# Optimization experiments

Measured on AMD Instinct MI355X. Metric: run time of the kernel, lower is better.

The kernel has to match this reference:

```python
import jax, jax.numpy as jnp
import numpy as np


def _gather_nbrs(feats, idx):
    # feats: [C, N], idx: [N, k] -> [C, N, k]
    return feats[:, idx]


def pointconv_dw(xyz, feats, idx, w_pos, b_pos, w_out, b_out):
    """Depthwise point conv: per-channel weights from relative neighbor coords.
    xyz: [B,3,N], feats: [B,C,N], idx: [B,N,k] -> [B,C_out,N]
    """
    nbr_xyz = jax.vmap(_gather_nbrs)(xyz, idx)            # [B,3,N,k]
    rel = nbr_xyz - xyz[:, :, :, None]                    # relative positions
    w = jnp.einsum('cd,bdnk->bcnk', w_pos, rel) + b_pos[None, :, None, None]
    g = jax.vmap(_gather_nbrs)(feats, idx)                # [B,C,N,k]
    agg = jnp.sum(w * g, axis=-1)                         # [B,C,N] depthwise reduce over k
    return jnp.einsum('oc,bcn->bon', w_out, agg) + b_out[None, :, None]


def setup_inputs() -> dict:
    key = jax.random.key(0)
    ks = jax.random.split(key, 16)
    B, N, K = 2, 65536, 4
    IN, HID = 64, 64
    C = HID + IN
    s = 0.02
    inp = {
        'xyz': jax.random.normal(ks[0], (B, 3, N), jnp.float32),
        'h': jax.random.normal(ks[1], (B, HID, N), jnp.float32),
        'x': jax.random.normal(ks[2], (B, IN, N), jnp.float32),
        'knn_indices': jax.random.randint(ks[3], (B, N, K), 0, N, jnp.int32),
    }
    names = ['z', 'r', 'q']
    for i, nm in enumerate(names):
        inp[f'w{nm}_pos'] = s * jax.random.normal(ks[4 + 4 * i], (C, 3), jnp.float32)
        inp[f'b{nm}_pos'] = jnp.zeros((C,), jnp.float32)
        inp[f'w{nm}_out'] = s * jax.random.normal(ks[5 + 4 * i], (HID, C), jnp.float32)
        inp[f'b{nm}_out'] = jnp.zeros((HID,), jnp.float32)
    return inp


def reference(xyz, h, x, knn_indices,
              wz_pos, bz_pos, wz_out, bz_out,
              wr_pos, br_pos, wr_out, br_out,
              wq_pos, bq_pos, wq_out, bq_out):
    hx = jnp.concatenate([h, x], axis=1)                  # [B, HID+IN, N]
    z = jax.nn.sigmoid(pointconv_dw(xyz, hx, knn_indices, wz_pos, bz_pos, wz_out, bz_out))
    r = jax.nn.sigmoid(pointconv_dw(xyz, hx, knn_indices, wr_pos, br_pos, wr_out, br_out))
    rhx = jnp.concatenate([r * h, x], axis=1)
    q = jnp.tanh(pointconv_dw(xyz, rhx, knn_indices, wq_pos, bq_pos, wq_out, bq_out))
    return (1.0 - z) * h + z * q
```

## Files before the change

### kernel.cpp

```cpp
#include <hip/hip_runtime.h>

#define NPTS 65536
#define BATCH 2
#define CCH 128
#define HIDC 64
#define LDA 136
#define ZLD 72

typedef unsigned short u16;
typedef __bf16 bf16_t;
typedef bf16_t bf16x8 __attribute__((ext_vector_type(8)));
typedef float f32x4 __attribute__((ext_vector_type(4)));

__device__ __forceinline__ u16 f2bf(float f){
  union { float f; unsigned u; } v; v.f = f;
  unsigned r = v.u + 0x7FFFu + ((v.u >> 16) & 1u);
  return (u16)(r >> 16);
}
__device__ __forceinline__ float bf2f(u16 u){
  union { unsigned u; float f; } v; v.u = ((unsigned)u) << 16; return v.f;
}
__device__ __forceinline__ float sigmoidf_(float v){ return 1.f/(1.f+__expf(-v)); }
__device__ __forceinline__ float tanhf_(float v){
  v = fminf(10.f, fmaxf(-10.f, v));
  float e = __expf(2.f*v);
  return (e-1.f)/(e+1.f);
}

__global__ __launch_bounds__(256) void kprep(const float* __restrict__ wz,
    const float* __restrict__ wr, const float* __restrict__ wq, u16* __restrict__ o){
  int i = blockIdx.x*256 + threadIdx.x;
  const float* s = (i < 8192) ? wz : ((i < 16384) ? wr : wq);
  o[i] = f2bf(s[i & 8191]);
}

__global__ __launch_bounds__(256) void k_pack(const float* __restrict__ h,
    const float* __restrict__ x, u16* __restrict__ hxT, u16* __restrict__ rhxT){
  int pn = blockIdx.x*256 + threadIdx.x;
  int b = pn >> 16;
  size_t fb = (size_t)b*HIDC*NPTS + (pn & 65535);
  size_t ob = (size_t)pn * CCH;
  u16 tmp[8];
  for (int c8 = 0; c8 < 8; ++c8){
    #pragma unroll
    for (int i = 0; i < 8; ++i) tmp[i] = f2bf(h[fb + (size_t)(c8*8+i)*NPTS]);
    uint4 v; __builtin_memcpy(&v, tmp, 16);
    *(uint4*)(hxT + ob + c8*8) = v;
  }
  for (int c8 = 0; c8 < 8; ++c8){
    #pragma unroll
    for (int i = 0; i < 8; ++i) tmp[i] = f2bf(x[fb + (size_t)(c8*8+i)*NPTS]);
    uint4 v; __builtin_memcpy(&v, tmp, 16);
    *(uint4*)(hxT + ob + 64 + c8*8) = v;
    *(uint4*)(rhxT + ob + 64 + c8*8) = v;
  }
}

__global__ __launch_bounds__(256) void k_zr(
    const float* __restrict__ xyz, const float* __restrict__ h,
    const int* __restrict__ knn,
    const float* __restrict__ wz_pos, const float* __restrict__ bz_pos,
    const float* __restrict__ bz_out,
    const float* __restrict__ wr_pos, const float* __restrict__ br_pos,
    const float* __restrict__ br_out,
    const u16* __restrict__ wzb, const u16* __restrict__ wrb,
    const u16* __restrict__ hxT, u16* __restrict__ rhxT, u16* __restrict__ z_ws)
{
  __shared__ __align__(16) u16 aggzT[64*LDA];
  __shared__ __align__(16) u16 aggrT[64*LDA];
  __shared__ __align__(16) u16 zst[64*ZLD];
  __shared__ float4 relk[256];
  __shared__ int jlds[256];
  __shared__ float4 wpz[128];
  __shared__ float4 wpr[128];

  int tid = threadIdx.x; int lane = tid & 63; int wv = tid >> 6;
  int bid = blockIdx.x; int b = bid >> 10; int n0 = (bid & 1023) << 6;
  size_t bN = (size_t)b * NPTS;

  {
    int p = tid >> 2, k = tid & 3;
    int j = knn[((bN + n0 + p) << 2) + k];
    jlds[tid] = j;
    const float* xb = xyz + (size_t)b*3*NPTS;
    float cx = xb[n0+p], cy = xb[NPTS + n0+p], cz = xb[2*NPTS + n0+p];
    relk[tid] = make_float4(xb[j]-cx, xb[NPTS+j]-cy, xb[2*NPTS+j]-cz, 0.f);
  }
  if (tid < 128){
    wpz[tid] = make_float4(wz_pos[tid*3], wz_pos[tid*3+1], wz_pos[tid*3+2], bz_pos[tid]);
  } else {
    int c = tid - 128;
    wpr[c] = make_float4(wr_pos[c*3], wr_pos[c*3+1], wr_pos[c*3+2], br_pos[c]);
  }
  __syncthreads();

  const u16* hxTb = hxT + (bN << 7);
  for (int i = 0; i < 32; ++i){
    int t = (i << 2) | wv;
    int p = t >> 1; int c = ((t & 1) << 6) | lane;
    float4 wz4 = wpz[c], wr4 = wpr[c];
    float az = 0.f, ar = 0.f;
    #pragma unroll
    for (int k = 0; k < 4; ++k){
      int j = jlds[(p << 2) | k];
      float g = bf2f(hxTb[((size_t)j << 7) | c]);
      float4 r = relk[(p << 2) | k];
      az += (wz4.w + wz4.x*r.x + wz4.y*r.y + wz4.z*r.z) * g;
      ar += (wr4.w + wr4.x*r.x + wr4.y*r.y + wr4.z*r.z) * g;
    }
    aggzT[p*LDA + c] = f2bf(az);
    aggrT[p*LDA + c] = f2bf(ar);
  }
  __syncthreads();

  int l15 = lane & 15, quad = lane >> 4;
  bf16x8 Az[4], Ar[4];
  #pragma unroll
  for (int s = 0; s < 4; ++s){
    Az[s] = *(const bf16x8*)(wzb + ((wv*16 + l15)*128 + s*32 + quad*8));
    Ar[s] = *(const bf16x8*)(wrb + ((wv*16 + l15)*128 + s*32 + quad*8));
  }
  f32x4 zero4 = {0.f,0.f,0.f,0.f};
  f32x4 accz[4], accr[4];
  #pragma unroll
  for (int nt = 0; nt < 4; ++nt){ accz[nt] = zero4; accr[nt] = zero4; }
  #pragma unroll
  for (int nt = 0; nt < 4; ++nt){
    #pragma unroll
    for (int s = 0; s < 4; ++s){
      bf16x8 bz = *(const bf16x8*)(aggzT + ((nt*16 + l15)*LDA + s*32 + quad*8));
      accz[nt] = __builtin_amdgcn_mfma_f32_16x16x32_bf16(Az[s], bz, accz[nt], 0, 0, 0);
    }
    #pragma unroll
    for (int s = 0; s < 4; ++s){
      bf16x8 br = *(const bf16x8*)(aggrT + ((nt*16 + l15)*LDA + s*32 + quad*8));
      accr[nt] = __builtin_amdgcn_mfma_f32_16x16x32_bf16(Ar[s], br, accr[nt], 0, 0, 0);
    }
  }
  __syncthreads();

  #pragma unroll
  for (int nt = 0; nt < 4; ++nt){
    #pragma unroll
    for (int reg = 0; reg < 4; ++reg){
      int o = (wv << 4) | (quad << 2) | reg;
      int p = (nt << 4) | l15;
      float zf = sigmoidf_(accz[nt][reg] + bz_out[o]);
      float rf = sigmoidf_(accr[nt][reg] + br_out[o]);
      float hv = h[(size_t)(b*HIDC + o)*NPTS + n0 + p];
      zst[o*ZLD + p] = f2bf(zf);
      aggzT[p*LDA + o] = f2bf(rf * hv);
    }
  }
  __syncthreads();

  for (int t = tid; t < 512; t += 256){
    int p = t >> 3, ch = (t & 7) << 3;
    uint4 v = *(const uint4*)(aggzT + p*LDA + ch);
    *(uint4*)(rhxT + ((bN + n0 + p) << 7) + ch) = v;
  }
  for (int t = tid; t < 512; t += 256){
    int o = t >> 3, ch = (t & 7) << 3;
    uint4 v = *(const uint4*)(zst + o*ZLD + ch);
    *(uint4*)(z_ws + (size_t)(b*HIDC + o)*NPTS + n0 + ch) = v;
  }
}

__global__ __launch_bounds__(256) void k_q(
    const float* __restrict__ xyz, const float* __restrict__ h,
    const int* __restrict__ knn,
    const float* __restrict__ wq_pos, const float* __restrict__ bq_pos,
    const float* __restrict__ bq_out,
    const u16* __restrict__ wqb, const u16* __restrict__ rhxT,
    const u16* __restrict__ z_ws, float* __restrict__ out)
{
  __shared__ __align__(16) u16 aggT[64*LDA];
  __shared__ float4 relk[256];
  __shared__ int jlds[256];
  __shared__ float4 wpq[128];

  int tid = threadIdx.x; int lane = tid & 63; int wv = tid >> 6;
  int bid = blockIdx.x; int b = bid >> 10; int n0 = (bid & 1023) << 6;
  size_t bN = (size_t)b * NPTS;

  {
    int p = tid >> 2, k = tid & 3;
    int j = knn[((bN + n0 + p) << 2) + k];
    jlds[tid] = j;
    const float* xb = xyz + (size_t)b*3*NPTS;
    float cx = xb[n0+p], cy = xb[NPTS + n0+p], cz = xb[2*NPTS + n0+p];
    relk[tid] = make_float4(xb[j]-cx, xb[NPTS+j]-cy, xb[2*NPTS+j]-cz, 0.f);
  }
  if (tid < 128){
    wpq[tid] = make_float4(wq_pos[tid*3], wq_pos[tid*3+1], wq_pos[tid*3+2], bq_pos[tid]);
  }
  __syncthreads();

  const u16* rhxTb = rhxT + (bN << 7);
  for (int i = 0; i < 32; ++i){
    int t = (i << 2) | wv;
    int p = t >> 1; int c = ((t & 1) << 6) | lane;
    float4 wq4 = wpq[c];
    float aq = 0.f;
    #pragma unroll
    for (int k = 0; k < 4; ++k){
      int j = jlds[(p << 2) | k];
      float g = bf2f(rhxTb[((size_t)j << 7) | c]);
      float4 r = relk[(p << 2) | k];
      aq += (wq4.w + wq4.x*r.x + wq4.y*r.y + wq4.z*r.z) * g;
    }
    aggT[p*LDA + c] = f2bf(aq);
  }
  __syncthreads();

  int l15 = lane & 15, quad = lane >> 4;
  bf16x8 Aq[4];
  #pragma unroll
  for (int s = 0; s < 4; ++s)
    Aq[s] = *(const bf16x8*)(wqb + ((wv*16 + l15)*128 + s*32 + quad*8));
  f32x4 zero4 = {0.f,0.f,0.f,0.f};
  f32x4 acc[4];
  #pragma unroll
  for (int nt = 0; nt < 4; ++nt) acc[nt] = zero4;
  #pragma unroll
  for (int nt = 0; nt < 4; ++nt){
    #pragma unroll
    for (int s = 0; s < 4; ++s){
      bf16x8 bq = *(const bf16x8*)(aggT + ((nt*16 + l15)*LDA + s*32 + quad*8));
      acc[nt] = __builtin_amdgcn_mfma_f32_16x16x32_bf16(Aq[s], bq, acc[nt], 0, 0, 0);
    }
  }

  #pragma unroll
  for (int nt = 0; nt < 4; ++nt){
    #pragma unroll
    for (int reg = 0; reg < 4; ++reg){
      int o = (wv << 4) | (quad << 2) | reg;
      int p = (nt << 4) | l15;
      size_t idx = (size_t)(b*HIDC + o)*NPTS + n0 + p;
      float qf = tanhf_(acc[nt][reg] + bq_out[o]);
      float zf = bf2f(z_ws[idx]);
      float hv = h[idx];
      out[idx] = (1.f - zf)*hv + zf*qf;
    }
  }
}

extern "C" void kernel_launch(void* const* d_in, const int* in_sizes, int n_in,
                              void* d_out, int out_size, void* d_ws, size_t ws_size,
                              hipStream_t stream){
  const float* xyz    = (const float*)d_in[0];
  const float* h      = (const float*)d_in[1];
  const float* x      = (const float*)d_in[2];
  const int*   knn    = (const int*)d_in[3];
  const float* wz_pos = (const float*)d_in[4];
  const float* bz_pos = (const float*)d_in[5];
  const float* wz_out = (const float*)d_in[6];
  const float* bz_out = (const float*)d_in[7];
  const float* wr_pos = (const float*)d_in[8];
  const float* br_pos = (const float*)d_in[9];
  const float* wr_out = (const float*)d_in[10];
  const float* br_out = (const float*)d_in[11];
  const float* wq_pos = (const float*)d_in[12];
  const float* bq_pos = (const float*)d_in[13];
  const float* wq_out = (const float*)d_in[14];
  const float* bq_out = (const float*)d_in[15];
  float* out = (float*)d_out;

  u16* ws   = (u16*)d_ws;
  u16* hxT  = ws;
  u16* rhxT = hxT + (size_t)BATCH*NPTS*CCH;
  u16* z_ws = rhxT + (size_t)BATCH*NPTS*CCH;
  u16* wbf  = z_ws + (size_t)BATCH*HIDC*NPTS;

  kprep<<<96, 256, 0, stream>>>(wz_out, wr_out, wq_out, wbf);
  k_pack<<<512, 256, 0, stream>>>(h, x, hxT, rhxT);
  k_zr<<<2048, 256, 0, stream>>>(xyz, h, knn, wz_pos, bz_pos, bz_out,
      wr_pos, br_pos, br_out, wbf, wbf + 8192, hxT, rhxT, z_ws);
  k_q<<<2048, 256, 0, stream>>>(xyz, h, knn, wq_pos, bq_pos, bq_out,
      wbf + 16384, rhxT, z_ws, out);
}
```

Baseline: 269.1 us.

## Fold position weights into output GEMM and vectorize neighbor gathers

Rewrites the depthwise position-weighted aggregation algebraically. Each point now keeps four moments per channel (sum of g, and x/y/z-weighted sums of g), giving a K=512 extended B matrix. The position coefficients are folded into the output weights in a prep kernel, so the per-channel weight computation becomes part of the MFMA GEMM. Gathers are vectorized as 16-byte loads per neighbor, the pack kernel transposes through LDS with coalesced float4 reads, and tiles shrink to 32 points per block with 4-block occupancy hints. The cost is four times more MFMA K-work and an extra bf16 rounding on the moments.

```diff
diff --git a/kernel.cpp b/kernel.cpp
--- a/kernel.cpp
+++ b/kernel.cpp
@@ -4,10 +4,12 @@
 #define BATCH 2
 #define CCH 128
 #define HIDC 64
-#define LDA 136
-#define ZLD 72
+#define PPB 32
+#define LDB 520
+#define PLD 136
 
 typedef unsigned short u16;
+typedef unsigned int u32;
 typedef __bf16 bf16_t;
 typedef bf16_t bf16x8 __attribute__((ext_vector_type(8)));
 typedef float f32x4 __attribute__((ext_vector_type(4)));
@@ -19,6 +21,10 @@
 }
 __device__ __forceinline__ float bf2f(u16 u){
   union { unsigned u; float f; } v; v.u = ((unsigned)u) << 16; return v.f;
+}
+__device__ __forceinline__ u32 pkrn(float a, float b){
+  union { float f; u32 u; } ua, ub; ua.f = a; ub.f = b;
+  return ((ua.u + 0x8000u) >> 16) | ((ub.u + 0x8000u) & 0xffff0000u);
 }
 __device__ __forceinline__ float sigmoidf_(float v){ return 1.f/(1.f+__expf(-v)); }
 __device__ __forceinline__ float tanhf_(float v){
@@ -27,217 +33,241 @@
   return (e-1.f)/(e+1.f);
 }
 
-__global__ __launch_bounds__(256) void kprep(const float* __restrict__ wz,
-    const float* __restrict__ wr, const float* __restrict__ wq, u16* __restrict__ o){
-  int i = blockIdx.x*256 + threadIdx.x;
-  const float* s = (i < 8192) ? wz : ((i < 16384) ? wr : wq);
-  o[i] = f2bf(s[i & 8191]);
+__global__ __launch_bounds__(256) void kprep(
+    const float* __restrict__ wz, const float* __restrict__ wzp, const float* __restrict__ bzp,
+    const float* __restrict__ wr, const float* __restrict__ wrp, const float* __restrict__ brp,
+    const float* __restrict__ wq, const float* __restrict__ wqp, const float* __restrict__ bqp,
+    u16* __restrict__ A){
+  int idx = blockIdx.x*256 + threadIdx.x;
+  int t = idx & 7, o = (idx>>3)&63, quad = (idx>>9)&3, s = (idx>>11)&15, g = idx>>15;
+  int pk = s*32 + quad*8 + t;
+  int j = pk>>7, chunk = (pk>>3)&15, tt = pk&7;
+  int orig = chunk*32 + j*8 + tt;
+  int c = orig>>2, m = orig&3;
+  const float* W  = (g==0)? wz  : (g==1)? wr  : wq;
+  const float* wp = (g==0)? wzp : (g==1)? wrp : wqp;
+  const float* bp = (g==0)? bzp : (g==1)? brp : bqp;
+  float coef = m ? wp[c*3 + m - 1] : bp[c];
+  A[idx] = f2bf(W[o*CCH + c] * coef);
 }
 
 __global__ __launch_bounds__(256) void k_pack(const float* __restrict__ h,
     const float* __restrict__ x, u16* __restrict__ hxT, u16* __restrict__ rhxT){
-  int pn = blockIdx.x*256 + threadIdx.x;
-  int b = pn >> 16;
-  size_t fb = (size_t)b*HIDC*NPTS + (pn & 65535);
-  size_t ob = (size_t)pn * CCH;
-  u16 tmp[8];
-  for (int c8 = 0; c8 < 8; ++c8){
-    #pragma unroll
-    for (int i = 0; i < 8; ++i) tmp[i] = f2bf(h[fb + (size_t)(c8*8+i)*NPTS]);
-    uint4 v; __builtin_memcpy(&v, tmp, 16);
-    *(uint4*)(hxT + ob + c8*8) = v;
-  }
-  for (int c8 = 0; c8 < 8; ++c8){
-    #pragma unroll
-    for (int i = 0; i < 8; ++i) tmp[i] = f2bf(x[fb + (size_t)(c8*8+i)*NPTS]);
-    uint4 v; __builtin_memcpy(&v, tmp, 16);
-    *(uint4*)(hxT + ob + 64 + c8*8) = v;
-    *(uint4*)(rhxT + ob + 64 + c8*8) = v;
-  }
-}
-
-__global__ __launch_bounds__(256) void k_zr(
+  __shared__ __align__(16) u16 tile[64*PLD];
+  int tid = threadIdx.x;
+  int b = blockIdx.x >> 10, n0 = (blockIdx.x & 1023) << 6;
+  #pragma unroll
+  for (int i = 0; i < 8; ++i){
+    int cc = (tid>>4) + i*16;
+    int nn = (tid & 15)*4;
+    const float* src = (cc < HIDC)
+        ? (h + (((size_t)(b*HIDC + cc))<<16) + n0 + nn)
+        : (x + (((size_t)(b*HIDC + cc - HIDC))<<16) + n0 + nn);
+    float4 v = *(const float4*)src;
+    tile[(nn+0)*PLD + cc] = f2bf(v.x);
+    tile[(nn+1)*PLD + cc] = f2bf(v.y);
+    tile[(nn+2)*PLD + cc] = f2bf(v.z);
+    tile[(nn+3)*PLD + cc] = f2bf(v.w);
+  }
+  __syncthreads();
+  #pragma unroll
+  for (int i = 0; i < 4; ++i){
+    int tsk = tid + (i<<8);
+    int n = tsk>>4, ch = (tsk&15)*8;
+    uint4 v = *(const uint4*)(tile + n*PLD + ch);
+    *(uint4*)(hxT + (((size_t)(b<<16) + n0 + n)<<7) + ch) = v;
+  }
+  #pragma unroll
+  for (int i = 0; i < 2; ++i){
+    int tsk = tid + (i<<8);
+    int n = tsk>>3, ch = HIDC + (tsk&7)*8;
+    uint4 v = *(const uint4*)(tile + n*PLD + ch);
+    *(uint4*)(rhxT + (((size_t)(b<<16) + n0 + n)<<7) + ch) = v;
+  }
+}
+
+#define ACCUM(gv, rv) { \
+  u32 dw_[4] = {gv.x, gv.y, gv.z, gv.w}; \
+  _Pragma("unroll") \
+  for (int q_ = 0; q_ < 4; ++q_){ \
+    union { u32 u; float f; } lo_, hi_; \
+    lo_.u = dw_[q_] << 16; hi_.u = dw_[q_] & 0xffff0000u; \
+    m0[2*q_]   += lo_.f; mx[2*q_]   += rv.x*lo_.f; my[2*q_]   += rv.y*lo_.f; mz[2*q_]   += rv.z*lo_.f; \
+    m0[2*q_+1] += hi_.f; mx[2*q_+1] += rv.x*hi_.f; my[2*q_+1] += rv.y*hi_.f; mz[2*q_+1] += rv.z*hi_.f; \
+  } }
+
+__global__ __launch_bounds__(256, 4) void k_zr(
     const float* __restrict__ xyz, const float* __restrict__ h,
     const int* __restrict__ knn,
-    const float* __restrict__ wz_pos, const float* __restrict__ bz_pos,
-    const float* __restrict__ bz_out,
-    const float* __restrict__ wr_pos, const float* __restrict__ br_pos,
-    const float* __restrict__ br_out,
-    const u16* __restrict__ wzb, const u16* __restrict__ wrb,
+    const float* __restrict__ bz_out, const float* __restrict__ br_out,
+    const u16* __restrict__ Azr,
     const u16* __restrict__ hxT, u16* __restrict__ rhxT, u16* __restrict__ z_ws)
 {
-  __shared__ __align__(16) u16 aggzT[64*LDA];
-  __shared__ __align__(16) u16 aggrT[64*LDA];
-  __shared__ __align__(16) u16 zst[64*ZLD];
-  __shared__ float4 relk[256];
-  __shared__ int jlds[256];
-  __shared__ float4 wpz[128];
-  __shared__ float4 wpr[128];
+  __shared__ __align__(16) u16 bext[PPB*LDB];
+  __shared__ __align__(16) float4 relk[PPB*4];
+  __shared__ __align__(16) int4 jlds[PPB];
 
   int tid = threadIdx.x; int lane = tid & 63; int wv = tid >> 6;
-  int bid = blockIdx.x; int b = bid >> 10; int n0 = (bid & 1023) << 6;
+  int b = blockIdx.x >> 11, n0 = (blockIdx.x & 2047) << 5;
   size_t bN = (size_t)b * NPTS;
 
-  {
+  if (tid < 128){
     int p = tid >> 2, k = tid & 3;
     int j = knn[((bN + n0 + p) << 2) + k];
-    jlds[tid] = j;
+    ((int*)jlds)[tid] = j;
     const float* xb = xyz + (size_t)b*3*NPTS;
     float cx = xb[n0+p], cy = xb[NPTS + n0+p], cz = xb[2*NPTS + n0+p];
     relk[tid] = make_float4(xb[j]-cx, xb[NPTS+j]-cy, xb[2*NPTS+j]-cz, 0.f);
   }
-  if (tid < 128){
-    wpz[tid] = make_float4(wz_pos[tid*3], wz_pos[tid*3+1], wz_pos[tid*3+2], bz_pos[tid]);
-  } else {
-    int c = tid - 128;
-    wpr[c] = make_float4(wr_pos[c*3], wr_pos[c*3+1], wr_pos[c*3+2], br_pos[c]);
-  }
   __syncthreads();
 
   const u16* hxTb = hxT + (bN << 7);
-  for (int i = 0; i < 32; ++i){
-    int t = (i << 2) | wv;
-    int p = t >> 1; int c = ((t & 1) << 6) | lane;
-    float4 wz4 = wpz[c], wr4 = wpr[c];
-    float az = 0.f, ar = 0.f;
-    #pragma unroll
-    for (int k = 0; k < 4; ++k){
-      int j = jlds[(p << 2) | k];
-      float g = bf2f(hxTb[((size_t)j << 7) | c]);
-      float4 r = relk[(p << 2) | k];
-      az += (wz4.w + wz4.x*r.x + wz4.y*r.y + wz4.z*r.z) * g;
-      ar += (wr4.w + wr4.x*r.x + wr4.y*r.y + wr4.z*r.z) * g;
-    }
-    aggzT[p*LDA + c] = f2bf(az);
-    aggrT[p*LDA + c] = f2bf(ar);
+  #pragma unroll
+  for (int it = 0; it < 2; ++it){
+    int task = tid + (it << 8);
+    int p = task >> 4, chunk = task & 15;
+    int4 jj = jlds[p];
+    uint4 g0 = *(const uint4*)(hxTb + (((size_t)jj.x)<<7) + chunk*8);
+    uint4 g1 = *(const uint4*)(hxTb + (((size_t)jj.y)<<7) + chunk*8);
+    uint4 g2 = *(const uint4*)(hxTb + (((size_t)jj.z)<<7) + chunk*8);
+    uint4 g3 = *(const uint4*)(hxTb + (((size_t)jj.w)<<7) + chunk*8);
+    float4 r0 = relk[p*4+0], r1 = relk[p*4+1], r2 = relk[p*4+2], r3 = relk[p*4+3];
+    float m0[8] = {0,0,0,0,0,0,0,0}, mx[8] = {0,0,0,0,0,0,0,0};
+    float my[8] = {0,0,0,0,0,0,0,0}, mz[8] = {0,0,0,0,0,0,0,0};
+    ACCUM(g0, r0); ACCUM(g1, r1); ACCUM(g2, r2); ACCUM(g3, r3);
+    u16* row = bext + p*LDB;
+    #pragma unroll
+    for (int j = 0; j < 4; ++j){
+      int ca = 2*j, cb = 2*j+1;
+      uint4 v;
+      v.x = pkrn(m0[ca], mx[ca]); v.y = pkrn(my[ca], mz[ca]);
+      v.z = pkrn(m0[cb], mx[cb]); v.w = pkrn(my[cb], mz[cb]);
+      *(uint4*)(row + j*128 + chunk*8) = v;
+    }
   }
   __syncthreads();
 
   int l15 = lane & 15, quad = lane >> 4;
-  bf16x8 Az[4], Ar[4];
-  #pragma unroll
-  for (int s = 0; s < 4; ++s){
-    Az[s] = *(const bf16x8*)(wzb + ((wv*16 + l15)*128 + s*32 + quad*8));
-    Ar[s] = *(const bf16x8*)(wrb + ((wv*16 + l15)*128 + s*32 + quad*8));
-  }
-  f32x4 zero4 = {0.f,0.f,0.f,0.f};
-  f32x4 accz[4], accr[4];
-  #pragma unroll
-  for (int nt = 0; nt < 4; ++nt){ accz[nt] = zero4; accr[nt] = zero4; }
-  #pragma unroll
-  for (int nt = 0; nt < 4; ++nt){
-    #pragma unroll
-    for (int s = 0; s < 4; ++s){
-      bf16x8 bz = *(const bf16x8*)(aggzT + ((nt*16 + l15)*LDA + s*32 + quad*8));
-      accz[nt] = __builtin_amdgcn_mfma_f32_16x16x32_bf16(Az[s], bz, accz[nt], 0, 0, 0);
-    }
-    #pragma unroll
-    for (int s = 0; s < 4; ++s){
-      bf16x8 br = *(const bf16x8*)(aggrT + ((nt*16 + l15)*LDA + s*32 + quad*8));
-      accr[nt] = __builtin_amdgcn_mfma_f32_16x16x32_bf16(Ar[s], br, accr[nt], 0, 0, 0);
-    }
-  }
-  __syncthreads();
-
-  #pragma unroll
-  for (int nt = 0; nt < 4; ++nt){
+  int orow = wv*16 + l15;
+  f32x4 accz[2], accr[2];
+  #pragma unroll
+  for (int nt = 0; nt < 2; ++nt){ accz[nt] = (f32x4){0,0,0,0}; accr[nt] = (f32x4){0,0,0,0}; }
+  #pragma unroll
+  for (int s = 0; s < 16; ++s){
+    bf16x8 az = *(const bf16x8*)(Azr + ((s*4 + quad)*64 + orow)*8);
+    bf16x8 ar = *(const bf16x8*)(Azr + 32768 + ((s*4 + quad)*64 + orow)*8);
+    #pragma unroll
+    for (int nt = 0; nt < 2; ++nt){
+      bf16x8 bb = *(const bf16x8*)(bext + (nt*16 + l15)*LDB + s*32 + quad*8);
+      accz[nt] = __builtin_amdgcn_mfma_f32_16x16x32_bf16(az, bb, accz[nt], 0, 0, 0);
+      accr[nt] = __builtin_amdgcn_mfma_f32_16x16x32_bf16(ar, bb, accr[nt], 0, 0, 0);
+    }
+  }
+  __syncthreads();
+
+  u16* zst  = bext;
+  u16* rhst = bext + 64*40;
+  #pragma unroll
+  for (int nt = 0; nt < 2; ++nt){
     #pragma unroll
     for (int reg = 0; reg < 4; ++reg){
-      int o = (wv << 4) | (quad << 2) | reg;
-      int p = (nt << 4) | l15;
+      int o = wv*16 + quad*4 + reg;
+      int p = nt*16 + l15;
       float zf = sigmoidf_(accz[nt][reg] + bz_out[o]);
       float rf = sigmoidf_(accr[nt][reg] + br_out[o]);
-      float hv = h[(size_t)(b*HIDC + o)*NPTS + n0 + p];
-      zst[o*ZLD + p] = f2bf(zf);
-      aggzT[p*LDA + o] = f2bf(rf * hv);
-    }
-  }
-  __syncthreads();
-
-  for (int t = tid; t < 512; t += 256){
-    int p = t >> 3, ch = (t & 7) << 3;
-    uint4 v = *(const uint4*)(aggzT + p*LDA + ch);
-    *(uint4*)(rhxT + ((bN + n0 + p) << 7) + ch) = v;
-  }
-  for (int t = tid; t < 512; t += 256){
-    int o = t >> 3, ch = (t & 7) << 3;
-    uint4 v = *(const uint4*)(zst + o*ZLD + ch);
-    *(uint4*)(z_ws + (size_t)(b*HIDC + o)*NPTS + n0 + ch) = v;
-  }
-}
-
-__global__ __launch_bounds__(256) void k_q(
+      float hv = h[(((size_t)(b*HIDC + o))<<16) + n0 + p];
+      zst[o*40 + p] = f2bf(zf);
+      rhst[p*72 + o] = f2bf(rf * hv);
+    }
+  }
+  __syncthreads();
+
+  {
+    int p = tid >> 3, ch = (tid & 7)*8;
+    uint4 v = *(const uint4*)(rhst + p*72 + ch);
+    *(uint4*)(rhxT + ((bN + n0 + p)<<7) + ch) = v;
+  }
+  {
+    int o = tid >> 2, pc = (tid & 3)*8;
+    uint4 v = *(const uint4*)(zst + o*40 + pc);
+    *(uint4*)(z_ws + (((size_t)(b*HIDC + o))<<16) + n0 + pc) = v;
+  }
+}
+
+__global__ __launch_bounds__(256, 4) void k_q(
     const float* __restrict__ xyz, const float* __restrict__ h,
     const int* __restrict__ knn,
-    const float* __restrict__ wq_pos, const float* __restrict__ bq_pos,
     const float* __restrict__ bq_out,
-    const u16* __restrict__ wqb, const u16* __restrict__ rhxT,
-    const u16* __restrict__ z_ws, float* __restrict__ out)
+    const u16* __restrict__ Aq,
+    const u16* __restrict__ rhxT, const u16* __restrict__ z_ws,
+    float* __restrict__ out)
 {
-  __shared__ __align__(16) u16 aggT[64*LDA];
-  __shared__ float4 relk[256];
-  __shared__ int jlds[256];
-  __shared__ float4 wpq[128];
+  __shared__ __align__(16) u16 bext[PPB*LDB];
+  __shared__ __align__(16) float4 relk[PPB*4];
+  __shared__ __align__(16) int4 jlds[PPB];
 
   int tid = threadIdx.x; int lane = tid & 63; int wv = tid >> 6;
-  int bid = blockIdx.x; int b = bid >> 10; int n0 = (bid & 1023) << 6;
+  int b = blockIdx.x >> 11, n0 = (blockIdx.x & 2047) << 5;
   size_t bN = (size_t)b * NPTS;
 
-  {
+  if (tid < 128){
     int p = tid >> 2, k = tid & 3;
     int j = knn[((bN + n0 + p) << 2) + k];
-    jlds[tid] = j;
+    ((int*)jlds)[tid] = j;
     const float* xb = xyz + (size_t)b*3*NPTS;
     float cx = xb[n0+p], cy = xb[NPTS + n0+p], cz = xb[2*NPTS + n0+p];
     relk[tid] = make_float4(xb[j]-cx, xb[NPTS+j]-cy, xb[2*NPTS+j]-cz, 0.f);
   }
-  if (tid < 128){
-    wpq[tid] = make_float4(wq_pos[tid*3], wq_pos[tid*3+1], wq_pos[tid*3+2], bq_pos[tid]);
-  }
   __syncthreads();
 
   const u16* rhxTb = rhxT + (bN << 7);
-  for (int i = 0; i < 32; ++i){
-    int t = (i << 2) | wv;
-    int p = t >> 1; int c = ((t & 1) << 6) | lane;
-    float4 wq4 = wpq[c];
-    float aq = 0.f;
-    #pragma unroll
-    for (int k = 0; k < 4; ++k){
-      int j = jlds[(p << 2) | k];
-      float g = bf2f(rhxTb[((size_t)j << 7) | c]);
-      float4 r = relk[(p << 2) | k];
-      aq += (wq4.w + wq4.x*r.x + wq4.y*r.y + wq4.z*r.z) * g;
-    }
-    aggT[p*LDA + c] = f2bf(aq);
+  #pragma unroll
+  for (int it = 0; it < 2; ++it){
+    int task = tid + (it << 8);
+    int p = task >> 4, chunk = task & 15;
+    int4 jj = jlds[p];
+    uint4 g0 = *(const uint4*)(rhxTb + (((size_t)jj.x)<<7) + chunk*8);
+    uint4 g1 = *(const uint4*)(rhxTb + (((size_t)jj.y)<<7) + chunk*8);
+    uint4 g2 = *(const uint4*)(rhxTb + (((size_t)jj.z)<<7) + chunk*8);
+    uint4 g3 = *(const uint4*)(rhxTb + (((size_t)jj.w)<<7) + chunk*8);
+    float4 r0 = relk[p*4+0], r1 = relk[p*4+1], r2 = relk[p*4+2], r3 = relk[p*4+3];
+    float m0[8] = {0,0,0,0,0,0,0,0}, mx[8] = {0,0,0,0,0,0,0,0};
+    float my[8] = {0,0,0,0,0,0,0,0}, mz[8] = {0,0,0,0,0,0,0,0};
+    ACCUM(g0, r0); ACCUM(g1, r1); ACCUM(g2, r2); ACCUM(g3, r3);
+    u16* row = bext + p*LDB;
+    #pragma unroll
+    for (int j = 0; j < 4; ++j){
+      int ca = 2*j, cb = 2*j+1;
+      uint4 v;
+      v.x = pkrn(m0[ca], mx[ca]); v.y = pkrn(my[ca], mz[ca]);
+      v.z = pkrn(m0[cb], mx[cb]); v.w = pkrn(my[cb], mz[cb]);
+      *(uint4*)(row + j*128 + chunk*8) = v;
+    }
   }
   __syncthreads();
 
   int l15 = lane & 15, quad = lane >> 4;
-  bf16x8 Aq[4];
-  #pragma unroll
-  for (int s = 0; s < 4; ++s)
-    Aq[s] = *(const bf16x8*)(wqb + ((wv*16 + l15)*128 + s*32 + quad*8));
-  f32x4 zero4 = {0.f,0.f,0.f,0.f};
-  f32x4 acc[4];
-  #pragma unroll
-  for (int nt = 0; nt < 4; ++nt) acc[nt] = zero4;
-  #pragma unroll
-  for (int nt = 0; nt < 4; ++nt){
-    #pragma unroll
-    for (int s = 0; s < 4; ++s){
-      bf16x8 bq = *(const bf16x8*)(aggT + ((nt*16 + l15)*LDA + s*32 + quad*8));
-      acc[nt] = __builtin_amdgcn_mfma_f32_16x16x32_bf16(Aq[s], bq, acc[nt], 0, 0, 0);
-    }
-  }
-
-  #pragma unroll
-  for (int nt = 0; nt < 4; ++nt){
+  int orow = wv*16 + l15;
+  f32x4 acc[2];
+  #pragma unroll
+  for (int nt = 0; nt < 2; ++nt) acc[nt] = (f32x4){0,0,0,0};
+  #pragma unroll
+  for (int s = 0; s < 16; ++s){
+    bf16x8 aq = *(const bf16x8*)(Aq + ((s*4 + quad)*64 + orow)*8);
+    #pragma unroll
+    for (int nt = 0; nt < 2; ++nt){
+      bf16x8 bb = *(const bf16x8*)(bext + (nt*16 + l15)*LDB + s*32 + quad*8);
+      acc[nt] = __builtin_amdgcn_mfma_f32_16x16x32_bf16(aq, bb, acc[nt], 0, 0, 0);
+    }
+  }
+
+  #pragma unroll
+  for (int nt = 0; nt < 2; ++nt){
     #pragma unroll
     for (int reg = 0; reg < 4; ++reg){
-      int o = (wv << 4) | (quad << 2) | reg;
-      int p = (nt << 4) | l15;
-      size_t idx = (size_t)(b*HIDC + o)*NPTS + n0 + p;
+      int o = wv*16 + quad*4 + reg;
+      int p = nt*16 + l15;
+      size_t idx = (((size_t)(b*HIDC + o))<<16) + n0 + p;
       float qf = tanhf_(acc[nt][reg] + bq_out[o]);
       float zf = bf2f(z_ws[idx]);
       float hv = h[idx];
@@ -271,12 +301,11 @@
   u16* hxT  = ws;
   u16* rhxT = hxT + (size_t)BATCH*NPTS*CCH;
   u16* z_ws = rhxT + (size_t)BATCH*NPTS*CCH;
-  u16* wbf  = z_ws + (size_t)BATCH*HIDC*NPTS;
-
-  kprep<<<96, 256, 0, stream>>>(wz_out, wr_out, wq_out, wbf);
-  k_pack<<<512, 256, 0, stream>>>(h, x, hxT, rhxT);
-  k_zr<<<2048, 256, 0, stream>>>(xyz, h, knn, wz_pos, bz_pos, bz_out,
-      wr_pos, br_pos, br_out, wbf, wbf + 8192, hxT, rhxT, z_ws);
-  k_q<<<2048, 256, 0, stream>>>(xyz, h, knn, wq_pos, bq_pos, bq_out,
-      wbf + 16384, rhxT, z_ws, out);
-}
+  u16* A    = z_ws + (size_t)BATCH*HIDC*NPTS;
+
+  kprep<<<384, 256, 0, stream>>>(wz_out, wz_pos, bz_pos, wr_out, wr_pos, br_pos,
+                                 wq_out, wq_pos, bq_pos, A);
+  k_pack<<<2048, 256, 0, stream>>>(h, x, hxT, rhxT);
+  k_zr<<<4096, 256, 0, stream>>>(xyz, h, knn, bz_out, br_out, A, hxT, rhxT, z_ws);
+  k_q<<<4096, 256, 0, stream>>>(xyz, h, knn, bq_out, A + 65536, rhxT, z_ws, out);
+}
```

Measured after the change: 234.9 us. -12.7%, faster.
